# Optimization experiments

Hardware: AMD Instinct MI355X
Metric: run time of the kernel (lower is better)

## Reference

```python
import jax, jax.numpy as jnp
import numpy as np


def _lstm_scan(x, w_ih, w_hh, b_ih, b_hh):
    """Unidirectional LSTM, PyTorch gate order (i, f, g, o).
    x: [B, T, C]; w_ih: [4H, C]; w_hh: [4H, H]. Returns [B, T, H]."""
    H = w_hh.shape[1]
    # Precompute input contribution for all timesteps (one big GEMM).
    xg = jnp.einsum('btc,gc->btg', x, w_ih) + b_ih + b_hh  # [B, T, 4H]

    def step(carry, xg_t):
        h, c = carry
        gates = xg_t + h @ w_hh.T
        i, f, g, o = jnp.split(gates, 4, axis=-1)
        c = jax.nn.sigmoid(f) * c + jax.nn.sigmoid(i) * jnp.tanh(g)
        h = jax.nn.sigmoid(o) * jnp.tanh(c)
        return (h, c), h

    B = x.shape[0]
    h0 = jnp.zeros((B, H), x.dtype)
    _, hs = jax.lax.scan(step, (h0, h0), jnp.swapaxes(xg, 0, 1))
    return jnp.swapaxes(hs, 0, 1)  # [B, T, H]


def _bilstm(x, w_ih_f, w_hh_f, b_ih_f, b_hh_f, w_ih_b, w_hh_b, b_ih_b, b_hh_b):
    fwd = _lstm_scan(x, w_ih_f, w_hh_f, b_ih_f, b_hh_f)
    bwd = _lstm_scan(x[:, ::-1], w_ih_b, w_hh_b, b_ih_b, b_hh_b)[:, ::-1]
    return jnp.concatenate([fwd, bwd], axis=-1)  # [B, T, 2H]


def setup_inputs() -> dict:
    key = jax.random.key(0)
    B, Hh, Ww, C, Hd = 64, 48, 48, 192, 48
    ks = jax.random.split(key, 20)
    s = 1.0 / np.sqrt(Hd)  # PyTorch LSTM init scale
    inp = {"x": jax.random.normal(ks[0], (B, Hh, Ww, C), jnp.float32)}
    names = ["v_w_ih_f", "v_w_hh_f", "v_b_ih_f", "v_b_hh_f",
             "v_w_ih_b", "v_w_hh_b", "v_b_ih_b", "v_b_hh_b",
             "h_w_ih_f", "h_w_hh_f", "h_b_ih_f", "h_b_hh_f",
             "h_w_ih_b", "h_w_hh_b", "h_b_ih_b", "h_b_hh_b"]
    shapes = [(4 * Hd, C), (4 * Hd, Hd), (4 * Hd,), (4 * Hd,)] * 4
    for i, (n, sh) in enumerate(zip(names, shapes)):
        inp[n] = jax.random.uniform(ks[1 + i], sh, jnp.float32, -s, s)
    inp["proj_w"] = jax.random.uniform(ks[17], (C, 4 * Hd), jnp.float32, -s, s)
    inp["proj_b"] = jax.random.uniform(ks[18], (C,), jnp.float32, -s, s)
    return inp


def reference(x, v_w_ih_f, v_w_hh_f, v_b_ih_f, v_b_hh_f,
              v_w_ih_b, v_w_hh_b, v_b_ih_b, v_b_hh_b,
              h_w_ih_f, h_w_hh_f, h_b_ih_f, h_b_hh_f,
              h_w_ih_b, h_w_hh_b, h_b_ih_b, h_b_hh_b,
              proj_w, proj_b):
    B, Hh, Ww, C = x.shape
    # Vertical: scan over height for each column.
    xv = jnp.transpose(x, (0, 2, 1, 3)).reshape(B * Ww, Hh, C)
    v = _bilstm(xv, v_w_ih_f, v_w_hh_f, v_b_ih_f, v_b_hh_f,
                v_w_ih_b, v_w_hh_b, v_b_ih_b, v_b_hh_b)
    v = jnp.transpose(v.reshape(B, Ww, Hh, -1), (0, 2, 1, 3))  # [B,H,W,2Hd]
    # Horizontal: scan over width for each row.
    xh = x.reshape(B * Hh, Ww, C)
    h = _bilstm(xh, h_w_ih_f, h_w_hh_f, h_b_ih_f, h_b_hh_f,
                h_w_ih_b, h_w_hh_b, h_b_ih_b, h_b_hh_b)
    h = h.reshape(B, Hh, Ww, -1)  # [B,H,W,2Hd]
    combined = jnp.concatenate([v, h], axis=-1)  # [B,H,W,4Hd]
    return jnp.einsum('bhwk,ck->bhwc', combined, proj_w) + proj_b
```

## Files before the change

### kernel.cpp

```cpp
#include <hip/hip_runtime.h>

typedef short short8 __attribute__((ext_vector_type(8)));
typedef short short4v __attribute__((ext_vector_type(4)));
typedef float f32x4 __attribute__((ext_vector_type(4)));
typedef unsigned short u16;

__device__ __forceinline__ u16 f2bf(float f) {
  unsigned int u = __builtin_bit_cast(unsigned int, f);
  u = (u + 0x7FFFu + ((u >> 16) & 1u)) >> 16;
  return (u16)u;
}
__device__ __forceinline__ short8 cvt8(float4 a, float4 b) {
  short8 v;
  v[0] = (short)f2bf(a.x); v[1] = (short)f2bf(a.y);
  v[2] = (short)f2bf(a.z); v[3] = (short)f2bf(a.w);
  v[4] = (short)f2bf(b.x); v[5] = (short)f2bf(b.y);
  v[6] = (short)f2bf(b.z); v[7] = (short)f2bf(b.w);
  return v;
}
__device__ __forceinline__ short8 cvt8s(float4 a, float4 b, float s) {
  short8 v;
  v[0] = (short)f2bf(a.x * s); v[1] = (short)f2bf(a.y * s);
  v[2] = (short)f2bf(a.z * s); v[3] = (short)f2bf(a.w * s);
  v[4] = (short)f2bf(b.x * s); v[5] = (short)f2bf(b.y * s);
  v[6] = (short)f2bf(b.z * s); v[7] = (short)f2bf(b.w * s);
  return v;
}

#define NPX 147456
#define L2E 1.44269504088896f

__global__ __launch_bounds__(256)
void xcvt_kernel(const float* __restrict__ x, u16* __restrict__ xbf)
{
  size_t c = ((size_t)blockIdx.x * 256 + threadIdx.x) * 8;
  const float4* p = (const float4*)(x + c);
  *(short8*)(xbf + c) = cvt8(p[0], p[1]);
}

__global__ __launch_bounds__(192)
void fused_scan_kernel(const u16* __restrict__ xbf,
    const float* __restrict__ wi0, const float* __restrict__ wi1,
    const float* __restrict__ wi2, const float* __restrict__ wi3,
    const float* __restrict__ u0, const float* __restrict__ u1,
    const float* __restrict__ u2, const float* __restrict__ u3,
    const float* __restrict__ bi0, const float* __restrict__ bh0,
    const float* __restrict__ bi1, const float* __restrict__ bh1,
    const float* __restrict__ bi2, const float* __restrict__ bh2,
    const float* __restrict__ bi3, const float* __restrict__ bh3,
    u16* __restrict__ comb)
{
  __shared__ u16 wl[36864];
  __shared__ u16 hs[3][1152];

  const int tid  = threadIdx.x;
  const int lane = tid & 63;
  const int wv   = tid >> 6;
  const int cl   = lane & 15;
  const int kg   = lane >> 4;
  const int dir  = blockIdx.x >> 6;
  const int sub  = blockIdx.x & 63;

  const float* wp  = dir == 0 ? wi0 : dir == 1 ? wi1 : dir == 2 ? wi2 : wi3;
  const float* up  = dir == 0 ? u0  : dir == 1 ? u1  : dir == 2 ? u2  : u3;
  const float* bip = dir == 0 ? bi0 : dir == 1 ? bi1 : dir == 2 ? bi2 : bi3;
  const float* bhp = dir == 0 ? bh0 : dir == 1 ? bh1 : dir == 2 ? bh2 : bh3;

  for (int i = 0; i < 24; ++i) {
    int ch  = tid + 192 * i;
    int row = ch / 24;
    int k0  = (ch % 24) * 8;
    float sc = (row >= 96 && row < 144) ? 2.0f * L2E : L2E;
    const float4* p = (const float4*)(wp + row * 192 + k0);
    *(short8*)&wl[(row * 192 + k0) ^ ((row & 7) << 3)] = cvt8s(p[0], p[1], sc);
  }

  short8 uf[12][2];
  #pragma unroll
  for (int nt = 0; nt < 12; ++nt) {
    int n = nt * 16 + cl;
    float sc = (n >= 96 && n < 144) ? 2.0f * L2E : L2E;
    {
      const float4* p = (const float4*)(up + n * 48 + kg * 8);
      uf[nt][0] = cvt8s(p[0], p[1], sc);
    }
    if (kg < 2) {
      const float4* p = (const float4*)(up + n * 48 + 32 + kg * 8);
      uf[nt][1] = cvt8s(p[0], p[1], sc);
    } else if (kg == 2) {
      short8 v = {};
      v[0] = (short)f2bf((bip[n] + bhp[n]) * sc);
      uf[nt][1] = v;
    } else {
      short8 z = {}; uf[nt][1] = z;
    }
  }

  #pragma unroll
  for (int i = 0; i < 18; ++i) {
    int idx = lane * 18 + i;
    hs[wv][idx] = (idx % 72 == 48) ? (u16)0x3F80 : (u16)0;
  }
  __syncthreads();

  const int W    = sub * 3 + wv;
  const int bb   = W / 3;
  const int rc   = (W - bb * 3) * 16 + cl;
  const bool vert = dir < 2;
  const bool bwd  = (dir & 1) != 0;
  const int tp0  = bwd ? 47 : 0;
  const int dpx  = (vert ? 48 : 1) * (bwd ? -1 : 1);
  const int px0  = vert ? (bb * 48 + tp0) * 48 + rc : (bb * 48 + rc) * 48 + tp0;

  const u16* xp = xbf + (size_t)px0 * 192 + kg * 8;
  const ptrdiff_t xstep = (ptrdiff_t)dpx * 192;

  short8 xf[6];
  #pragma unroll
  for (int kk = 0; kk < 6; ++kk) xf[kk] = *(const short8*)(xp + kk * 32);

  f32x4 c0 = {0.f,0.f,0.f,0.f}, c1 = c0, c2 = c0;
  u16* cbp = comb + ((size_t)dir * NPX + px0) * 48 + kg * 4;
  const ptrdiff_t cstep = (ptrdiff_t)dpx * 48;

  const int swz = (cl & 7) << 3;

  for (int t = 0; t < 48; ++t) {
    short8 hb0 = *(const short8*)&hs[wv][cl * 72 + kg * 8];
    short8 hb1 = *(const short8*)&hs[wv][cl * 72 + 32 + kg * 8];

    f32x4 acc[12];
    #pragma unroll
    for (int nt = 0; nt < 12; ++nt) acc[nt] = (f32x4){0.f,0.f,0.f,0.f};

    #pragma unroll
    for (int kk = 0; kk < 6; ++kk) {
      short8 w[6];
      #pragma unroll
      for (int nt = 0; nt < 6; ++nt)
        w[nt] = *(const short8*)&wl[((nt * 16 + cl) * 192 + kk * 32 + kg * 8) ^ swz];
      #pragma unroll
      for (int nt = 0; nt < 6; ++nt)
        acc[nt] = __builtin_amdgcn_mfma_f32_16x16x32_bf16(w[nt], xf[kk], acc[nt], 0, 0, 0);
      #pragma unroll
      for (int nt = 0; nt < 6; ++nt)
        w[nt] = *(const short8*)&wl[(((nt + 6) * 16 + cl) * 192 + kk * 32 + kg * 8) ^ swz];
      #pragma unroll
      for (int nt = 0; nt < 6; ++nt)
        acc[nt + 6] = __builtin_amdgcn_mfma_f32_16x16x32_bf16(w[nt], xf[kk], acc[nt + 6], 0, 0, 0);
    }

    if (t < 47) {
      xp += xstep;
      #pragma unroll
      for (int kk = 0; kk < 6; ++kk) xf[kk] = *(const short8*)(xp + kk * 32);
    }

    #pragma unroll
    for (int nt = 0; nt < 12; ++nt)
      acc[nt] = __builtin_amdgcn_mfma_f32_16x16x32_bf16(uf[nt][0], hb0, acc[nt], 0, 0, 0);
    #pragma unroll
    for (int nt = 0; nt < 12; ++nt)
      acc[nt] = __builtin_amdgcn_mfma_f32_16x16x32_bf16(uf[nt][1], hb1, acc[nt], 0, 0, 0);

    #pragma unroll
    for (int q = 0; q < 3; ++q) {
      f32x4& cq = q == 0 ? c0 : q == 1 ? c1 : c2;
      short4v h4;
      #pragma unroll
      for (int r = 0; r < 4; ++r) {
        float ii = __builtin_amdgcn_rcpf(1.0f + __builtin_exp2f(-acc[q][r]));
        float ff = __builtin_amdgcn_rcpf(1.0f + __builtin_exp2f(-acc[3 + q][r]));
        float gg = 1.0f - 2.0f * __builtin_amdgcn_rcpf(1.0f + __builtin_exp2f(acc[6 + q][r]));
        float oo = __builtin_amdgcn_rcpf(1.0f + __builtin_exp2f(-acc[9 + q][r]));
        float cc = ff * cq[r] + ii * gg;
        cq[r] = cc;
        float th = 1.0f - 2.0f * __builtin_amdgcn_rcpf(1.0f + __builtin_exp2f(cc * (2.0f * L2E)));
        h4[r] = (short)f2bf(oo * th);
      }
      *(short4v*)&hs[wv][cl * 72 + q * 16 + kg * 4] = h4;
      *(short4v*)(cbp + q * 16) = h4;
    }
    cbp += cstep;
  }
}

__global__ __launch_bounds__(256)
void proj_kernel(const u16* __restrict__ comb,
                 const float* __restrict__ pw,
                 const float* __restrict__ pb,
                 float* __restrict__ out)
{
  __shared__ u16 al[12288];
  const int tid  = threadIdx.x;
  const int lane = tid & 63;
  const int wv   = tid >> 6;
  const int cl   = lane & 15;
  const int kg   = lane >> 4;
  const int pxb  = blockIdx.x * 64;

  #pragma unroll
  for (int i = 0; i < 6; ++i) {
    int ch = tid + 256 * i;
    int pxl = ch / 24;
    int kk0 = (ch % 24) << 3;
    int d   = kk0 / 48;
    short8 v = *(const short8*)(comb + ((size_t)d * NPX + pxb + pxl) * 48 + (kk0 - d * 48));
    *(short8*)&al[(pxl * 192 + kk0) ^ ((pxl & 7) << 3)] = v;
  }

  short8 wf[3][6];
  #pragma unroll
  for (int nt = 0; nt < 3; ++nt) {
    int n = wv * 48 + nt * 16 + cl;
    #pragma unroll
    for (int kk = 0; kk < 6; ++kk) {
      const float4* p = (const float4*)(pw + n * 192 + kk * 32 + kg * 8);
      wf[nt][kk] = cvt8(p[0], p[1]);
    }
  }
  f32x4 bvv[3];
  #pragma unroll
  for (int nt = 0; nt < 3; ++nt)
    #pragma unroll
    for (int r = 0; r < 4; ++r)
      bvv[nt][r] = pb[wv * 48 + nt * 16 + kg * 4 + r];

  __syncthreads();

  f32x4 acc[3][4];
  #pragma unroll
  for (int nt = 0; nt < 3; ++nt)
    #pragma unroll
    for (int mi = 0; mi < 4; ++mi) acc[nt][mi] = bvv[nt];

  #pragma unroll
  for (int kk = 0; kk < 6; ++kk) {
    short8 bfr[4];
    #pragma unroll
    for (int mi = 0; mi < 4; ++mi) {
      int row = mi * 16 + cl;
      bfr[mi] = *(const short8*)&al[(row * 192 + kk * 32 + kg * 8) ^ ((row & 7) << 3)];
    }
    #pragma unroll
    for (int nt = 0; nt < 3; ++nt)
      #pragma unroll
      for (int mi = 0; mi < 4; ++mi)
        acc[nt][mi] = __builtin_amdgcn_mfma_f32_16x16x32_bf16(wf[nt][kk], bfr[mi], acc[nt][mi], 0, 0, 0);
  }

  #pragma unroll
  for (int nt = 0; nt < 3; ++nt)
    #pragma unroll
    for (int mi = 0; mi < 4; ++mi) {
      size_t o = (size_t)(pxb + mi * 16 + cl) * 192 + wv * 48 + nt * 16 + kg * 4;
      *(f32x4*)(out + o) = acc[nt][mi];
    }
}

extern "C" void kernel_launch(void* const* d_in, const int* in_sizes, int n_in,
                              void* d_out, int out_size, void* d_ws, size_t ws_size,
                              hipStream_t stream) {
  const float* x = (const float*)d_in[0];
  u16* xbf  = (u16*)d_ws;
  u16* comb = (u16*)d_ws + (size_t)NPX * 192;

  xcvt_kernel<<<13824, 256, 0, stream>>>(x, xbf);

  fused_scan_kernel<<<256, 192, 0, stream>>>(
      xbf,
      (const float*)d_in[1], (const float*)d_in[5],
      (const float*)d_in[9], (const float*)d_in[13],
      (const float*)d_in[2], (const float*)d_in[6],
      (const float*)d_in[10], (const float*)d_in[14],
      (const float*)d_in[3],  (const float*)d_in[4],
      (const float*)d_in[7],  (const float*)d_in[8],
      (const float*)d_in[11], (const float*)d_in[12],
      (const float*)d_in[15], (const float*)d_in[16],
      comb);

  proj_kernel<<<2304, 256, 0, stream>>>(
      comb, (const float*)d_in[17], (const float*)d_in[18], (float*)d_out);
}
```

Before: 256.7 us.

## Process two timesteps per iteration to reuse LDS weight loads for input projection

```diff
diff --git a/kernel.cpp b/kernel.cpp
--- a/kernel.cpp
+++ b/kernel.cpp
@@ -38,7 +38,7 @@
   *(short8*)(xbf + c) = cvt8(p[0], p[1]);
 }
 
-__global__ __launch_bounds__(192)
+__global__ __launch_bounds__(192, 1)
 void fused_scan_kernel(const u16* __restrict__ xbf,
     const float* __restrict__ wi0, const float* __restrict__ wi1,
     const float* __restrict__ wi2, const float* __restrict__ wi3,
@@ -112,26 +112,28 @@
   const int dpx  = (vert ? 48 : 1) * (bwd ? -1 : 1);
   const int px0  = vert ? (bb * 48 + tp0) * 48 + rc : (bb * 48 + rc) * 48 + tp0;
 
+  const ptrdiff_t xstep = (ptrdiff_t)dpx * 192;
   const u16* xp = xbf + (size_t)px0 * 192 + kg * 8;
-  const ptrdiff_t xstep = (ptrdiff_t)dpx * 192;
-
-  short8 xf[6];
-  #pragma unroll
-  for (int kk = 0; kk < 6; ++kk) xf[kk] = *(const short8*)(xp + kk * 32);
+
+  short8 xfA[6], xfB[6];
+  #pragma unroll
+  for (int kk = 0; kk < 6; ++kk) xfA[kk] = *(const short8*)(xp + kk * 32);
+  #pragma unroll
+  for (int kk = 0; kk < 6; ++kk) xfB[kk] = *(const short8*)(xp + xstep + kk * 32);
+  const u16* xpn = xp + 2 * xstep;
 
   f32x4 c0 = {0.f,0.f,0.f,0.f}, c1 = c0, c2 = c0;
   u16* cbp = comb + ((size_t)dir * NPX + px0) * 48 + kg * 4;
   const ptrdiff_t cstep = (ptrdiff_t)dpx * 48;
-
   const int swz = (cl & 7) << 3;
 
-  for (int t = 0; t < 48; ++t) {
+  for (int it = 0; it < 24; ++it) {
     short8 hb0 = *(const short8*)&hs[wv][cl * 72 + kg * 8];
     short8 hb1 = *(const short8*)&hs[wv][cl * 72 + 32 + kg * 8];
 
-    f32x4 acc[12];
-    #pragma unroll
-    for (int nt = 0; nt < 12; ++nt) acc[nt] = (f32x4){0.f,0.f,0.f,0.f};
+    f32x4 aT[12], aU[12];
+    #pragma unroll
+    for (int nt = 0; nt < 12; ++nt) { aT[nt] = (f32x4){0.f,0.f,0.f,0.f}; aU[nt] = aT[nt]; }
 
     #pragma unroll
     for (int kk = 0; kk < 6; ++kk) {
@@ -140,28 +142,34 @@
       for (int nt = 0; nt < 6; ++nt)
         w[nt] = *(const short8*)&wl[((nt * 16 + cl) * 192 + kk * 32 + kg * 8) ^ swz];
       #pragma unroll
-      for (int nt = 0; nt < 6; ++nt)
-        acc[nt] = __builtin_amdgcn_mfma_f32_16x16x32_bf16(w[nt], xf[kk], acc[nt], 0, 0, 0);
+      for (int nt = 0; nt < 6; ++nt) {
+        aT[nt] = __builtin_amdgcn_mfma_f32_16x16x32_bf16(w[nt], xfA[kk], aT[nt], 0, 0, 0);
+        aU[nt] = __builtin_amdgcn_mfma_f32_16x16x32_bf16(w[nt], xfB[kk], aU[nt], 0, 0, 0);
+      }
       #pragma unroll
       for (int nt = 0; nt < 6; ++nt)
         w[nt] = *(const short8*)&wl[(((nt + 6) * 16 + cl) * 192 + kk * 32 + kg * 8) ^ swz];
       #pragma unroll
-      for (int nt = 0; nt < 6; ++nt)
-        acc[nt + 6] = __builtin_amdgcn_mfma_f32_16x16x32_bf16(w[nt], xf[kk], acc[nt + 6], 0, 0, 0);
-    }
-
-    if (t < 47) {
-      xp += xstep;
-      #pragma unroll
-      for (int kk = 0; kk < 6; ++kk) xf[kk] = *(const short8*)(xp + kk * 32);
+      for (int nt = 0; nt < 6; ++nt) {
+        aT[nt + 6] = __builtin_amdgcn_mfma_f32_16x16x32_bf16(w[nt], xfA[kk], aT[nt + 6], 0, 0, 0);
+        aU[nt + 6] = __builtin_amdgcn_mfma_f32_16x16x32_bf16(w[nt], xfB[kk], aU[nt + 6], 0, 0, 0);
+      }
+    }
+
+    if (it < 23) {
+      #pragma unroll
+      for (int kk = 0; kk < 6; ++kk) xfA[kk] = *(const short8*)(xpn + kk * 32);
+      #pragma unroll
+      for (int kk = 0; kk < 6; ++kk) xfB[kk] = *(const short8*)(xpn + xstep + kk * 32);
+      xpn += 2 * xstep;
     }
 
     #pragma unroll
     for (int nt = 0; nt < 12; ++nt)
-      acc[nt] = __builtin_amdgcn_mfma_f32_16x16x32_bf16(uf[nt][0], hb0, acc[nt], 0, 0, 0);
+      aT[nt] = __builtin_amdgcn_mfma_f32_16x16x32_bf16(uf[nt][0], hb0, aT[nt], 0, 0, 0);
     #pragma unroll
     for (int nt = 0; nt < 12; ++nt)
-      acc[nt] = __builtin_amdgcn_mfma_f32_16x16x32_bf16(uf[nt][1], hb1, acc[nt], 0, 0, 0);
+      aT[nt] = __builtin_amdgcn_mfma_f32_16x16x32_bf16(uf[nt][1], hb1, aT[nt], 0, 0, 0);
 
     #pragma unroll
     for (int q = 0; q < 3; ++q) {
@@ -169,10 +177,40 @@
       short4v h4;
       #pragma unroll
       for (int r = 0; r < 4; ++r) {
-        float ii = __builtin_amdgcn_rcpf(1.0f + __builtin_exp2f(-acc[q][r]));
-        float ff = __builtin_amdgcn_rcpf(1.0f + __builtin_exp2f(-acc[3 + q][r]));
-        float gg = 1.0f - 2.0f * __builtin_amdgcn_rcpf(1.0f + __builtin_exp2f(acc[6 + q][r]));
-        float oo = __builtin_amdgcn_rcpf(1.0f + __builtin_exp2f(-acc[9 + q][r]));
+        float ii = __builtin_amdgcn_rcpf(1.0f + __builtin_exp2f(-aT[q][r]));
+        float ff = __builtin_amdgcn_rcpf(1.0f + __builtin_exp2f(-aT[3 + q][r]));
+        float gg = 1.0f - 2.0f * __builtin_amdgcn_rcpf(1.0f + __builtin_exp2f(aT[6 + q][r]));
+        float oo = __builtin_amdgcn_rcpf(1.0f + __builtin_exp2f(-aT[9 + q][r]));
+        float cc = ff * cq[r] + ii * gg;
+        cq[r] = cc;
+        float th = 1.0f - 2.0f * __builtin_amdgcn_rcpf(1.0f + __builtin_exp2f(cc * (2.0f * L2E)));
+        h4[r] = (short)f2bf(oo * th);
+      }
+      *(short4v*)&hs[wv][cl * 72 + q * 16 + kg * 4] = h4;
+      *(short4v*)(cbp + q * 16) = h4;
+    }
+    cbp += cstep;
+
+    short8 hb0b = *(const short8*)&hs[wv][cl * 72 + kg * 8];
+    short8 hb1b = *(const short8*)&hs[wv][cl * 72 + 32 + kg * 8];
+
+    #pragma unroll
+    for (int nt = 0; nt < 12; ++nt)
+      aU[nt] = __builtin_amdgcn_mfma_f32_16x16x32_bf16(uf[nt][0], hb0b, aU[nt], 0, 0, 0);
+    #pragma unroll
+    for (int nt = 0; nt < 12; ++nt)
+      aU[nt] = __builtin_amdgcn_mfma_f32_16x16x32_bf16(uf[nt][1], hb1b, aU[nt], 0, 0, 0);
+
+    #pragma unroll
+    for (int q = 0; q < 3; ++q) {
+      f32x4& cq = q == 0 ? c0 : q == 1 ? c1 : c2;
+      short4v h4;
+      #pragma unroll
+      for (int r = 0; r < 4; ++r) {
+        float ii = __builtin_amdgcn_rcpf(1.0f + __builtin_exp2f(-aU[q][r]));
+        float ff = __builtin_amdgcn_rcpf(1.0f + __builtin_exp2f(-aU[3 + q][r]));
+        float gg = 1.0f - 2.0f * __builtin_amdgcn_rcpf(1.0f + __builtin_exp2f(aU[6 + q][r]));
+        float oo = __builtin_amdgcn_rcpf(1.0f + __builtin_exp2f(-aU[9 + q][r]));
         float cc = ff * cq[r] + ii * gg;
         cq[r] = cc;
         float th = 1.0f - 2.0f * __builtin_amdgcn_rcpf(1.0f + __builtin_exp2f(cc * (2.0f * L2E)));
```

Measured after the change: 361.8 us. 1.41x slower.
